# Optimization experiments

Measured on AMD Instinct MI355X. Metric: run time of the kernel, lower is better.

The kernel has to match this reference:

```python
import jax, jax.numpy as jnp
import numpy as np

B, C, H, W = 16, 256, 128, 128
C4, COUT = C // 4, 256


def setup_inputs() -> dict:
    key = jax.random.key(0)
    ks = jax.random.split(key, 8)
    s = 0.05
    flow = jax.random.normal(ks[0], (B, C, H, W), jnp.float32)
    de_out = jax.random.normal(ks[1], (B, C, H, W), jnp.float32)
    Wq = jax.random.normal(ks[2], (C4, C), jnp.float32) * s
    bq = jax.random.normal(ks[3], (C4,), jnp.float32) * s
    Wk = jax.random.normal(ks[4], (C4, C), jnp.float32) * s
    bk = jax.random.normal(ks[5], (C4,), jnp.float32) * s
    Wv = jax.random.normal(ks[6], (COUT, C), jnp.float32) * s
    bv = jax.random.normal(ks[7], (COUT,), jnp.float32) * s
    return {"flow": flow, "de_out": de_out, "Wq": Wq, "bq": bq,
            "Wk": Wk, "bk": bk, "Wv": Wv, "bv": bv}


def reference(flow, de_out, Wq, bq, Wk, bk, Wv, bv):
    # 1x1 convs == per-pixel channel matmuls
    q = jnp.einsum('bchw,dc->bdhw', de_out, Wq) + bq[None, :, None, None]  # [B,C4,H,W]
    k = jnp.einsum('bchw,dc->bdhw', flow, Wk) + bk[None, :, None, None]    # [B,C4,H,W]
    v = jnp.einsum('bchw,dc->bdhw', flow, Wv) + bv[None, :, None, None]    # [B,COUT,H,W]
    # height-axis attention per (batch, width) column
    energy = jnp.einsum('bdhw,bdgw->bwhg', q, k)          # [B,W,H,H], g = key height
    att = jax.nn.softmax(energy, axis=-1)                  # softmax over key height
    out = jnp.einsum('bcgw,bwhg->bchw', v, att)            # [B,COUT,H,W]
    return out
```

## Files before the change

### kernel.cpp

```cpp
#include <hip/hip_runtime.h>
#include <cstdint>
#include <cstddef>

typedef unsigned short u16;
using half4 = __attribute__((ext_vector_type(4))) _Float16;
using half8 = __attribute__((ext_vector_type(8))) _Float16;
using f32x4 = __attribute__((ext_vector_type(4))) float;
using f4    = __attribute__((ext_vector_type(4))) float;

#define B_    16
#define C_    256
#define H_    128
#define W_    128
#define C4_   64
#define COUT_ 256
#define HW_   (H_ * W_)

#define LDS_S1    264
#define QK_S      72
#define P_S       136
#define XP_S      140
#define O_S       72

#define Q_ELEMS   ((size_t)B_ * W_ * H_ * C4_)
#define V_ELEMS   ((size_t)B_ * W_ * H_ * COUT_)
#define W16_ELEMS ((size_t)(C4_ * C_ + C4_ * C_ + COUT_ * C_))
#define WS_NEED   ((2 * Q_ELEMS + 2 * V_ELEMS + W16_ELEMS) * 2)

__device__ __forceinline__ u16 f16_rn(float f) {
  _Float16 h = (_Float16)f;
  return __builtin_bit_cast(u16, h);
}

__device__ __forceinline__ void gload16(const void* g, void* l) {
  __builtin_amdgcn_global_load_lds(
      (const __attribute__((address_space(1))) void*)g,
      (__attribute__((address_space(3))) void*)l, 16, 0, 0);
}

__global__ void __launch_bounds__(256) wconv_kernel(
    const float* __restrict__ Wk, const float* __restrict__ Wq,
    const float* __restrict__ Wv, u16* __restrict__ W16) {
  const int bid = blockIdx.x;
  const int t   = threadIdx.x;
  const float* src;
  u16* dst;
  int idx;
  if (bid < 16)      { src = Wk; dst = W16;                 idx = bid * 1024 + t * 4; }
  else if (bid < 32) { src = Wq; dst = W16 + C4_ * C_;      idx = (bid - 16) * 1024 + t * 4; }
  else               { src = Wv; dst = W16 + 2 * C4_ * C_;  idx = (bid - 32) * 1024 + t * 4; }
  f4 v = *reinterpret_cast<const f4*>(src + idx);
  half4 h;
#pragma unroll
  for (int i = 0; i < 4; ++i) h[i] = (_Float16)v[i];
  *reinterpret_cast<half4*>(dst + idx) = h;
}

__device__ __forceinline__ const half8* afrag(const u16* __restrict__ T,
                                              int w16, int ks, int lg) {
  int oct = (ks * 4 + lg) ^ ((w16 >> 2) & 7);
  return reinterpret_cast<const half8*>(&T[w16 * LDS_S1 + oct * 8]);
}

__device__ __forceinline__ const half8* whfrag(const u16* __restrict__ Wm16,
                                               int row, int ks, int lg) {
  return reinterpret_cast<const half8*>(Wm16 + (size_t)row * C_ + ks * 32 + lg * 8);
}

__global__ void __launch_bounds__(256, 3) qkv_kernel(
    const float* __restrict__ flow, const float* __restrict__ de_out,
    const u16* __restrict__ W16,
    const float* __restrict__ bq, const float* __restrict__ bk,
    const float* __restrict__ bv,
    u16* __restrict__ Qws, u16* __restrict__ Kws, u16* __restrict__ Vws) {
  __shared__ __align__(16) unsigned char ldsraw[16384 + 64 * LDS_S1 * 2];
  float* F = reinterpret_cast<float*>(ldsraw);
  u16*   T = reinterpret_cast<u16*>(ldsraw + 16384);
  u16*   O = reinterpret_cast<u16*>(ldsraw);

  const int t    = threadIdx.x;
  const int bid  = blockIdx.x;
  const int g      = (bid & 7) | ((bid >> 6) << 3);
  const int hlow   = (bid >> 3) & 7;
  const int w0     = (g & 1) * 64;
  const int hgrp   = (g >> 1) & 15;
  const int b      = (g >> 5) & 15;
  const int srcsel = g >> 9;
  const int h      = hgrp * 8 + hlow;
  const int lane = t & 63;
  const int wv   = t >> 6;
  const int col  = lane & 15;
  const int lg   = lane >> 4;

  const u16* Wk16 = W16;
  const u16* Wq16 = W16 + C4_ * C_;
  const u16* Wv16 = W16 + 2 * C4_ * C_;

  const float* src =
      (srcsel ? de_out : flow) + (size_t)b * C_ * HW_ + (size_t)h * W_ + w0;

  for (int qtr = 0; qtr < 4; ++qtr) {
    const float* s = src + (size_t)(qtr * 64) * HW_;
#pragma unroll
    for (int i = 0; i < 4; ++i) {
      const int rr0 = wv * 16 + i * 4;
      gload16(s + (size_t)(rr0 + (lane >> 4)) * HW_ + (lane & 15) * 4,
              F + rr0 * 64);
    }
    __syncthreads();
#pragma unroll
    for (int i = 0; i < 2; ++i) {
      const int flat = i * 256 + t;
      const int wq = flat & 15;
      const int pp = flat >> 4;
      const f4 fa = *reinterpret_cast<const f4*>(&F[(2 * pp) * 64 + wq * 4]);
      const f4 fb = *reinterpret_cast<const f4*>(&F[(2 * pp + 1) * 64 + wq * 4]);
      const int c   = qtr * 64 + 2 * pp;
      const int oct = (c >> 3) ^ (wq & 7);
#pragma unroll
      for (int j = 0; j < 4; ++j) {
        const int w = wq * 4 + j;
        uint32_t pk = (uint32_t)f16_rn(fa[j]) | ((uint32_t)f16_rn(fb[j]) << 16);
        *reinterpret_cast<uint32_t*>(&T[w * LDS_S1 + oct * 8 + (c & 7)]) = pk;
      }
    }
    __syncthreads();
  }

  if (srcsel == 0) {
    f32x4 zero = {0.f, 0.f, 0.f, 0.f};
    {
      f32x4 acc[4];
#pragma unroll
      for (int i = 0; i < 4; ++i) acc[i] = zero;
#pragma unroll
      for (int ks = 0; ks < 8; ++ks) {
        const half8 bfr = *whfrag(Wk16, wv * 16 + col, ks, lg);
#pragma unroll
        for (int wt = 0; wt < 4; ++wt) {
          const half8 afr = *afrag(T, wt * 16 + col, ks, lg);
          acc[wt] = __builtin_amdgcn_mfma_f32_16x16x32_f16(afr, bfr, acc[wt], 0, 0, 0);
        }
      }
      const float bias = bk[wv * 16 + col];
#pragma unroll
      for (int wt = 0; wt < 4; ++wt)
#pragma unroll
        for (int r = 0; r < 4; ++r)
          O[(wt * 16 + lg * 4 + r) * O_S + wv * 16 + col] = f16_rn(acc[wt][r] + bias);
    }
    __syncthreads();
    {
#pragma unroll
      for (int i = 0; i < 2; ++i) {
        const int item = i * 256 + t;
        const int wl = item >> 3;
        const int d0 = (item & 7) * 8;
        *reinterpret_cast<half8*>(
            &Kws[(((size_t)b * W_ + w0 + wl) * H_ + h) * C4_ + d0]) =
            *reinterpret_cast<const half8*>(&O[wl * O_S + d0]);
      }
    }
    f32x4 acc[4][4];
#pragma unroll
    for (int j = 0; j < 4; ++j)
#pragma unroll
      for (int i = 0; i < 4; ++i) acc[j][i] = zero;
#pragma unroll
    for (int ks = 0; ks < 8; ++ks) {
      half8 bfr[4];
#pragma unroll
      for (int j = 0; j < 4; ++j)
        bfr[j] = *whfrag(Wv16, (wv * 4 + j) * 16 + col, ks, lg);
#pragma unroll
      for (int wt = 0; wt < 4; ++wt) {
        const half8 afr = *afrag(T, wt * 16 + col, ks, lg);
#pragma unroll
        for (int j = 0; j < 4; ++j)
          acc[j][wt] =
              __builtin_amdgcn_mfma_f32_16x16x32_f16(afr, bfr[j], acc[j][wt], 0, 0, 0);
      }
    }
#pragma unroll
    for (int j = 0; j < 4; ++j) {
      const int co = (wv * 4 + j) * 16 + col;
      const float bias = bv[co];
#pragma unroll
      for (int wt = 0; wt < 4; ++wt)
#pragma unroll
        for (int r = 0; r < 4; ++r) {
          int w = w0 + wt * 16 + lg * 4 + r;
          Vws[(size_t)(b * W_ + w) * 32768 + ((h >> 3) * COUT_ + co) * 8 + (h & 7)] =
              f16_rn(acc[j][wt][r] + bias);
        }
    }
  } else {
    f32x4 zero = {0.f, 0.f, 0.f, 0.f};
    f32x4 acc[4];
#pragma unroll
    for (int i = 0; i < 4; ++i) acc[i] = zero;
#pragma unroll
    for (int ks = 0; ks < 8; ++ks) {
      const half8 bfr = *whfrag(Wq16, wv * 16 + col, ks, lg);
#pragma unroll
      for (int wt = 0; wt < 4; ++wt) {
        const half8 afr = *afrag(T, wt * 16 + col, ks, lg);
        acc[wt] = __builtin_amdgcn_mfma_f32_16x16x32_f16(afr, bfr, acc[wt], 0, 0, 0);
      }
    }
    const float bias = bq[wv * 16 + col];
#pragma unroll
    for (int wt = 0; wt < 4; ++wt)
#pragma unroll
      for (int r = 0; r < 4; ++r)
        O[(wt * 16 + lg * 4 + r) * O_S + wv * 16 + col] = f16_rn(acc[wt][r] + bias);
    __syncthreads();
    {
#pragma unroll
      for (int i = 0; i < 2; ++i) {
        const int item = i * 256 + t;
        const int wl = item >> 3;
        const int d0 = (item & 7) * 8;
        *reinterpret_cast<half8*>(
            &Qws[(((size_t)b * W_ + w0 + wl) * H_ + h) * C4_ + d0]) =
            *reinterpret_cast<const half8*>(&O[wl * O_S + d0]);
      }
    }
  }
}

template <int EPI>
__global__ void __launch_bounds__(256) attn_kernel(
    const u16* __restrict__ Qws, const u16* __restrict__ Kws,
    const u16* __restrict__ Vws, u16* __restrict__ out_tmp,
    float* __restrict__ out) {
  __shared__ __align__(16) u16 ldsQK[2 * 128 * QK_S];

  const int t   = threadIdx.x;
  const int bid = blockIdx.x;
  const int sw  = (bid & 7) * 256 + (bid >> 3);
  const int b   = sw >> 7;
  const int w   = sw & 127;
  const int lane = t & 63;
  const int wv   = t >> 6;
  const int col  = lane & 15;
  const int lg   = lane >> 4;

  const u16* qc    = Qws + ((size_t)b * W_ + w) * H_ * C4_;
  const u16* kc    = Kws + ((size_t)b * W_ + w) * H_ * C4_;
  const u16* vbase = Vws + (size_t)(b * W_ + w) * 32768;

  u16* ldsQ = ldsQK;
  u16* ldsK = ldsQK + 128 * QK_S;

#pragma unroll
  for (int i = 0; i < 4; ++i) {
    int item = i * 256 + t;
    int hh   = item >> 3;
    int d0   = (item & 7) * 8;
    *reinterpret_cast<half8*>(&ldsQ[hh * QK_S + d0]) =
        *reinterpret_cast<const half8*>(qc + item * 8);
    *reinterpret_cast<half8*>(&ldsK[hh * QK_S + d0]) =
        *reinterpret_cast<const half8*>(kc + item * 8);
  }
  __syncthreads();

  f32x4 zero = {0.f, 0.f, 0.f, 0.f};
  f32x4 e[2][8];
#pragma unroll
  for (int ht = 0; ht < 2; ++ht)
#pragma unroll
    for (int gt = 0; gt < 8; ++gt) e[ht][gt] = zero;

#pragma unroll
  for (int ks = 0; ks < 2; ++ks) {
    half8 aq[2];
#pragma unroll
    for (int ht = 0; ht < 2; ++ht)
      aq[ht] = *reinterpret_cast<const half8*>(
          &ldsQ[(wv * 32 + ht * 16 + col) * QK_S + ks * 32 + lg * 8]);
#pragma unroll
    for (int gt = 0; gt < 8; ++gt) {
      const half8 bk_ = *reinterpret_cast<const half8*>(
          &ldsK[(gt * 16 + col) * QK_S + ks * 32 + lg * 8]);
#pragma unroll
      for (int ht = 0; ht < 2; ++ht)
        e[ht][gt] = __builtin_amdgcn_mfma_f32_16x16x32_f16(aq[ht], bk_, e[ht][gt], 0, 0, 0);
    }
  }
  __syncthreads();

  u16* ldsP = ldsQK + wv * 32 * P_S;

#pragma unroll
  for (int ht = 0; ht < 2; ++ht)
#pragma unroll
    for (int r = 0; r < 4; ++r) {
      float m = -1e30f;
#pragma unroll
      for (int gt = 0; gt < 8; ++gt) m = fmaxf(m, e[ht][gt][r]);
#pragma unroll
      for (int off = 1; off < 16; off <<= 1) m = fmaxf(m, __shfl_xor(m, off));
      float s = 0.f;
#pragma unroll
      for (int gt = 0; gt < 8; ++gt) {
        float p = __expf(e[ht][gt][r] - m);
        e[ht][gt][r] = p;
        s += p;
      }
#pragma unroll
      for (int off = 1; off < 16; off <<= 1) s += __shfl_xor(s, off);
      const float inv = 1.f / s;
      const int hh = ht * 16 + lg * 4 + r;
#pragma unroll
      for (int gt = 0; gt < 8; ++gt)
        ldsP[hh * P_S + gt * 16 + col] = f16_rn(e[ht][gt][r] * inv);
    }

  f32x4 o[2][16];
#pragma unroll
  for (int ht = 0; ht < 2; ++ht)
#pragma unroll
    for (int ct = 0; ct < 16; ++ct) o[ht][ct] = zero;

#pragma unroll
  for (int ks = 0; ks < 4; ++ks) {
    half8 ap[2];
#pragma unroll
    for (int ht = 0; ht < 2; ++ht)
      ap[ht] = *reinterpret_cast<const half8*>(
          &ldsP[(ht * 16 + col) * P_S + ks * 32 + lg * 8]);
#pragma unroll
    for (int ct = 0; ct < 16; ++ct) {
      const half8 bv_ = *reinterpret_cast<const half8*>(
          vbase + ((ks * 4 + lg) * COUT_ + ct * 16 + col) * 8);
#pragma unroll
      for (int ht = 0; ht < 2; ++ht)
        o[ht][ct] = __builtin_amdgcn_mfma_f32_16x16x32_f16(ap[ht], bv_, o[ht][ct], 0, 0, 0);
    }
  }

  if (EPI == 1) {
    u16* ldsX = ldsQK;
    u16* dst_col = out_tmp + ((size_t)(b * W_ + w) << 15);
#pragma unroll
    for (int ctg = 0; ctg < 4; ++ctg) {
      __syncthreads();
#pragma unroll
      for (int j = 0; j < 4; ++j) {
        const int ct    = ctg * 4 + j;
        const int c_loc = j * 16 + col;
#pragma unroll
        for (int ht = 0; ht < 2; ++ht) {
          const int hbase = wv * 32 + ht * 16 + lg * 4;
          half4 pk;
#pragma unroll
          for (int r = 0; r < 4; ++r) pk[r] = (_Float16)o[ht][ct][r];
          *reinterpret_cast<half4*>(&ldsX[c_loc * XP_S + hbase]) = pk;
        }
      }
      __syncthreads();
      const int c_loc = t >> 2;
      const int h0    = (t & 3) * 32;
      u16* dp = dst_col + (ctg * 64 + c_loc) * 128 + h0;
#pragma unroll
      for (int k = 0; k < 4; ++k)
        *reinterpret_cast<half8*>(dp + k * 8) =
            *reinterpret_cast<const half8*>(&ldsX[c_loc * XP_S + h0 + k * 8]);
    }
  } else {
    float* outp = out + (size_t)b * COUT_ * HW_ + w;
#pragma unroll
    for (int ht = 0; ht < 2; ++ht)
#pragma unroll
      for (int ct = 0; ct < 16; ++ct)
#pragma unroll
        for (int r = 0; r < 4; ++r) {
          int hrow = wv * 32 + ht * 16 + lg * 4 + r;
          int c = ct * 16 + col;
          outp[((size_t)c * H_ + hrow) * W_] = o[ht][ct][r];
        }
  }
}

__global__ void __launch_bounds__(256) transpose_kernel(
    const u16* __restrict__ T, float* __restrict__ out) {
  __shared__ float lds[64 * 132];
  const int t   = threadIdx.x;
  const int bid = blockIdx.x;
  const int b   = bid >> 9;
  const int ft  = bid & 511;

  {
    const int w  = t >> 1;
    const int fo = (t & 1) * 32;
    const u16* src = T + ((size_t)(b * W_ + w) << 15) + ft * 64 + fo;
#pragma unroll
    for (int k = 0; k < 4; ++k) {
      half8 v = *reinterpret_cast<const half8*>(src + k * 8);
#pragma unroll
      for (int e = 0; e < 8; ++e)
        lds[(fo + k * 8 + e) * 132 + w] = (float)v[e];
    }
  }
  __syncthreads();
  {
    const int f_loc = t >> 2;
    const int w0    = (t & 3) * 32;
    float* dst = out + (size_t)b * (COUT_ * HW_) + (size_t)(ft * 64 + f_loc) * 128 + w0;
#pragma unroll
    for (int k = 0; k < 8; ++k) {
      f4 v4;
#pragma unroll
      for (int e = 0; e < 4; ++e) v4[e] = lds[f_loc * 132 + w0 + k * 4 + e];
      *reinterpret_cast<f4*>(dst + k * 4) = v4;
    }
  }
}

extern "C" void kernel_launch(void* const* d_in, const int* in_sizes, int n_in,
                              void* d_out, int out_size, void* d_ws, size_t ws_size,
                              hipStream_t stream) {
  const float* flow   = (const float*)d_in[0];
  const float* de_out = (const float*)d_in[1];
  const float* Wq = (const float*)d_in[2];
  const float* bq = (const float*)d_in[3];
  const float* Wk = (const float*)d_in[4];
  const float* bk = (const float*)d_in[5];
  const float* Wv = (const float*)d_in[6];
  const float* bv = (const float*)d_in[7];
  float* out = (float*)d_out;

  u16* Qws = (u16*)d_ws;
  u16* Kws = Qws + Q_ELEMS;
  u16* Vws = Kws + Q_ELEMS;
  u16* W16 = Vws + V_ELEMS;
  u16* Tws = W16 + W16_ELEMS;

  wconv_kernel<<<96, 256, 0, stream>>>(Wk, Wq, Wv, W16);
  qkv_kernel<<<2 * B_ * H_ * 2, 256, 0, stream>>>(flow, de_out, W16, bq, bk, bv,
                                                  Qws, Kws, Vws);
  if (ws_size >= (size_t)WS_NEED) {
    attn_kernel<1><<<B_ * W_, 256, 0, stream>>>(Qws, Kws, Vws, Tws, out);
    transpose_kernel<<<B_ * 512, 256, 0, stream>>>(Tws, out);
  } else {
    attn_kernel<0><<<B_ * W_, 256, 0, stream>>>(Qws, Kws, Vws, Tws, out);
  }
}
```

Measured before the change: 547.6 us.

## Double-buffer QKV input loads and interleave MFMA with channel-quarter staging

Restructures the QKV projection kernel so each 64-channel quarter of the input is prefetched into a second LDS buffer while the current quarter is converted to fp16 and immediately consumed by MFMAs. Accumulation over K now happens per quarter instead of after the whole 256-channel tile is staged, which shrinks the transposed tile from 256 to 64 channels per row. The aim is to hide global-load latency behind conversion and matrix math. In exchange, LDS grows to hold two float buffers, and the K and V accumulators are live at the same time across the loop, which raises register pressure and may reduce occupancy. Synchronisation uses hand-written waitcnt and barrier asm.

```diff
diff --git a/kernel.cpp b/kernel.cpp
--- a/kernel.cpp
+++ b/kernel.cpp
@@ -16,7 +16,7 @@
 #define COUT_ 256
 #define HW_   (H_ * W_)
 
-#define LDS_S1    264
+#define T_S       72
 #define QK_S      72
 #define P_S       136
 #define XP_S      140
@@ -56,10 +56,10 @@
   *reinterpret_cast<half4*>(dst + idx) = h;
 }
 
-__device__ __forceinline__ const half8* afrag(const u16* __restrict__ T,
-                                              int w16, int ks, int lg) {
-  int oct = (ks * 4 + lg) ^ ((w16 >> 2) & 7);
-  return reinterpret_cast<const half8*>(&T[w16 * LDS_S1 + oct * 8]);
+__device__ __forceinline__ const half8* afragq(const u16* __restrict__ T,
+                                               int w16, int ksl, int lg) {
+  int oct = (ksl * 4 + lg) ^ ((w16 >> 2) & 7);
+  return reinterpret_cast<const half8*>(&T[w16 * T_S + oct * 8]);
 }
 
 __device__ __forceinline__ const half8* whfrag(const u16* __restrict__ Wm16,
@@ -73,10 +73,11 @@
     const float* __restrict__ bq, const float* __restrict__ bk,
     const float* __restrict__ bv,
     u16* __restrict__ Qws, u16* __restrict__ Kws, u16* __restrict__ Vws) {
-  __shared__ __align__(16) unsigned char ldsraw[16384 + 64 * LDS_S1 * 2];
-  float* F = reinterpret_cast<float*>(ldsraw);
-  u16*   T = reinterpret_cast<u16*>(ldsraw + 16384);
-  u16*   O = reinterpret_cast<u16*>(ldsraw);
+  __shared__ __align__(16) unsigned char ldsraw[2 * 16384 + 64 * T_S * 2];
+  float* Fbuf[2] = {reinterpret_cast<float*>(ldsraw),
+                    reinterpret_cast<float*>(ldsraw + 16384)};
+  u16* T = reinterpret_cast<u16*>(ldsraw + 32768);
+  u16* O = reinterpret_cast<u16*>(ldsraw);
 
   const int t    = threadIdx.x;
   const int bid  = blockIdx.x;
@@ -99,58 +100,99 @@
   const float* src =
       (srcsel ? de_out : flow) + (size_t)b * C_ * HW_ + (size_t)h * W_ + w0;
 
-  for (int qtr = 0; qtr < 4; ++qtr) {
-    const float* s = src + (size_t)(qtr * 64) * HW_;
-#pragma unroll
-    for (int i = 0; i < 4; ++i) {
-      const int rr0 = wv * 16 + i * 4;
-      gload16(s + (size_t)(rr0 + (lane >> 4)) * HW_ + (lane & 15) * 4,
-              F + rr0 * 64);
-    }
-    __syncthreads();
+  f32x4 zero = {0.f, 0.f, 0.f, 0.f};
+  f32x4 acc0[4];
+  f32x4 accV[4][4];
+#pragma unroll
+  for (int i = 0; i < 4; ++i) acc0[i] = zero;
+#pragma unroll
+  for (int j = 0; j < 4; ++j)
+#pragma unroll
+    for (int i = 0; i < 4; ++i) accV[j][i] = zero;
+
+#pragma unroll
+  for (int i = 0; i < 4; ++i) {
+    const int rr0 = wv * 16 + i * 4;
+    gload16(src + (size_t)(rr0 + (lane >> 4)) * HW_ + (lane & 15) * 4,
+            Fbuf[0] + rr0 * 64);
+  }
+
+#pragma unroll
+  for (int q = 0; q < 4; ++q) {
+    float* Fc = Fbuf[q & 1];
+    float* Fn = Fbuf[(q + 1) & 1];
+    if (q < 3) {
+      const float* s = src + (size_t)((q + 1) * 64) * HW_;
+#pragma unroll
+      for (int i = 0; i < 4; ++i) {
+        const int rr0 = wv * 16 + i * 4;
+        gload16(s + (size_t)(rr0 + (lane >> 4)) * HW_ + (lane & 15) * 4,
+                Fn + rr0 * 64);
+      }
+      asm volatile("s_waitcnt vmcnt(4) lgkmcnt(0)\ns_barrier" ::: "memory");
+    } else {
+      asm volatile("s_waitcnt vmcnt(0) lgkmcnt(0)\ns_barrier" ::: "memory");
+    }
+    __builtin_amdgcn_sched_barrier(0);
+
 #pragma unroll
     for (int i = 0; i < 2; ++i) {
       const int flat = i * 256 + t;
       const int wq = flat & 15;
       const int pp = flat >> 4;
-      const f4 fa = *reinterpret_cast<const f4*>(&F[(2 * pp) * 64 + wq * 4]);
-      const f4 fb = *reinterpret_cast<const f4*>(&F[(2 * pp + 1) * 64 + wq * 4]);
-      const int c   = qtr * 64 + 2 * pp;
-      const int oct = (c >> 3) ^ (wq & 7);
+      const f4 fa = *reinterpret_cast<const f4*>(&Fc[(2 * pp) * 64 + wq * 4]);
+      const f4 fb = *reinterpret_cast<const f4*>(&Fc[(2 * pp + 1) * 64 + wq * 4]);
+      const int c_loc = 2 * pp;
+      const int oct   = (c_loc >> 3) ^ (wq & 7);
 #pragma unroll
       for (int j = 0; j < 4; ++j) {
         const int w = wq * 4 + j;
         uint32_t pk = (uint32_t)f16_rn(fa[j]) | ((uint32_t)f16_rn(fb[j]) << 16);
-        *reinterpret_cast<uint32_t*>(&T[w * LDS_S1 + oct * 8 + (c & 7)]) = pk;
-      }
-    }
-    __syncthreads();
+        *reinterpret_cast<uint32_t*>(&T[w * T_S + oct * 8 + (c_loc & 7)]) = pk;
+      }
+    }
+    asm volatile("s_waitcnt lgkmcnt(0)\ns_barrier" ::: "memory");
+    __builtin_amdgcn_sched_barrier(0);
+
+#pragma unroll
+    for (int ksl = 0; ksl < 2; ++ksl) {
+      const int ks = 2 * q + ksl;
+      if (srcsel == 0) {
+        const half8 bK = *whfrag(Wk16, wv * 16 + col, ks, lg);
+        half8 bV[4];
+#pragma unroll
+        for (int j = 0; j < 4; ++j)
+          bV[j] = *whfrag(Wv16, (wv * 4 + j) * 16 + col, ks, lg);
+#pragma unroll
+        for (int wt = 0; wt < 4; ++wt) {
+          const half8 afr = *afragq(T, wt * 16 + col, ksl, lg);
+          acc0[wt] = __builtin_amdgcn_mfma_f32_16x16x32_f16(afr, bK, acc0[wt], 0, 0, 0);
+#pragma unroll
+          for (int j = 0; j < 4; ++j)
+            accV[j][wt] =
+                __builtin_amdgcn_mfma_f32_16x16x32_f16(afr, bV[j], accV[j][wt], 0, 0, 0);
+        }
+      } else {
+        const half8 bQ = *whfrag(Wq16, wv * 16 + col, ks, lg);
+#pragma unroll
+        for (int wt = 0; wt < 4; ++wt) {
+          const half8 afr = *afragq(T, wt * 16 + col, ksl, lg);
+          acc0[wt] = __builtin_amdgcn_mfma_f32_16x16x32_f16(afr, bQ, acc0[wt], 0, 0, 0);
+        }
+      }
+    }
   }
 
   if (srcsel == 0) {
-    f32x4 zero = {0.f, 0.f, 0.f, 0.f};
     {
-      f32x4 acc[4];
-#pragma unroll
-      for (int i = 0; i < 4; ++i) acc[i] = zero;
-#pragma unroll
-      for (int ks = 0; ks < 8; ++ks) {
-        const half8 bfr = *whfrag(Wk16, wv * 16 + col, ks, lg);
-#pragma unroll
-        for (int wt = 0; wt < 4; ++wt) {
-          const half8 afr = *afrag(T, wt * 16 + col, ks, lg);
-          acc[wt] = __builtin_amdgcn_mfma_f32_16x16x32_f16(afr, bfr, acc[wt], 0, 0, 0);
-        }
-      }
       const float bias = bk[wv * 16 + col];
+      __syncthreads();
 #pragma unroll
       for (int wt = 0; wt < 4; ++wt)
 #pragma unroll
         for (int r = 0; r < 4; ++r)
-          O[(wt * 16 + lg * 4 + r) * O_S + wv * 16 + col] = f16_rn(acc[wt][r] + bias);
-    }
-    __syncthreads();
-    {
+          O[(wt * 16 + lg * 4 + r) * O_S + wv * 16 + col] = f16_rn(acc0[wt][r] + bias);
+      __syncthreads();
 #pragma unroll
       for (int i = 0; i < 2; ++i) {
         const int item = i * 256 + t;
@@ -161,26 +203,6 @@
             *reinterpret_cast<const half8*>(&O[wl * O_S + d0]);
       }
     }
-    f32x4 acc[4][4];
-#pragma unroll
-    for (int j = 0; j < 4; ++j)
-#pragma unroll
-      for (int i = 0; i < 4; ++i) acc[j][i] = zero;
-#pragma unroll
-    for (int ks = 0; ks < 8; ++ks) {
-      half8 bfr[4];
-#pragma unroll
-      for (int j = 0; j < 4; ++j)
-        bfr[j] = *whfrag(Wv16, (wv * 4 + j) * 16 + col, ks, lg);
-#pragma unroll
-      for (int wt = 0; wt < 4; ++wt) {
-        const half8 afr = *afrag(T, wt * 16 + col, ks, lg);
-#pragma unroll
-        for (int j = 0; j < 4; ++j)
-          acc[j][wt] =
-              __builtin_amdgcn_mfma_f32_16x16x32_f16(afr, bfr[j], acc[j][wt], 0, 0, 0);
-      }
-    }
 #pragma unroll
     for (int j = 0; j < 4; ++j) {
       const int co = (wv * 4 + j) * 16 + col;
@@ -191,40 +213,26 @@
         for (int r = 0; r < 4; ++r) {
           int w = w0 + wt * 16 + lg * 4 + r;
           Vws[(size_t)(b * W_ + w) * 32768 + ((h >> 3) * COUT_ + co) * 8 + (h & 7)] =
-              f16_rn(acc[j][wt][r] + bias);
+              f16_rn(accV[j][wt][r] + bias);
         }
     }
   } else {
-    f32x4 zero = {0.f, 0.f, 0.f, 0.f};
-    f32x4 acc[4];
-#pragma unroll
-    for (int i = 0; i < 4; ++i) acc[i] = zero;
-#pragma unroll
-    for (int ks = 0; ks < 8; ++ks) {
-      const half8 bfr = *whfrag(Wq16, wv * 16 + col, ks, lg);
-#pragma unroll
-      for (int wt = 0; wt < 4; ++wt) {
-        const half8 afr = *afrag(T, wt * 16 + col, ks, lg);
-        acc[wt] = __builtin_amdgcn_mfma_f32_16x16x32_f16(afr, bfr, acc[wt], 0, 0, 0);
-      }
-    }
     const float bias = bq[wv * 16 + col];
+    __syncthreads();
 #pragma unroll
     for (int wt = 0; wt < 4; ++wt)
 #pragma unroll
       for (int r = 0; r < 4; ++r)
-        O[(wt * 16 + lg * 4 + r) * O_S + wv * 16 + col] = f16_rn(acc[wt][r] + bias);
+        O[(wt * 16 + lg * 4 + r) * O_S + wv * 16 + col] = f16_rn(acc0[wt][r] + bias);
     __syncthreads();
-    {
-#pragma unroll
-      for (int i = 0; i < 2; ++i) {
-        const int item = i * 256 + t;
-        const int wl = item >> 3;
-        const int d0 = (item & 7) * 8;
-        *reinterpret_cast<half8*>(
-            &Qws[(((size_t)b * W_ + w0 + wl) * H_ + h) * C4_ + d0]) =
-            *reinterpret_cast<const half8*>(&O[wl * O_S + d0]);
-      }
+#pragma unroll
+    for (int i = 0; i < 2; ++i) {
+      const int item = i * 256 + t;
+      const int wl = item >> 3;
+      const int d0 = (item & 7) * 8;
+      *reinterpret_cast<half8*>(
+          &Qws[(((size_t)b * W_ + w0 + wl) * H_ + h) * C4_ + d0]) =
+          *reinterpret_cast<const half8*>(&O[wl * O_S + d0]);
     }
   }
 }
```

New measurement: 539.1 us. No clear change (-1.6%).
